# Kernel tuning notes

Measured on AMD Instinct MI355X. Metric: run time of the kernel, lower is better.

The kernel has to match this reference:

```python
import jax, jax.numpy as jnp
import numpy as np
import math

SPARSITY = 0.95


def _linear(x, W, b):
    # torch nn.Linear: y = x @ W.T + b, W is [out, in]
    return jnp.einsum('bsd,od->bso', x, W) + b


def setup_inputs() -> dict:
    key = jax.random.key(0)
    ks = jax.random.split(key, 11)
    B, S, D = 2, 4096, 512
    std = 1.0 / math.sqrt(D)
    inp = {
        'x': jax.random.normal(ks[0], (B, S, D), dtype=jnp.float32),
        'mask_rand': jax.random.uniform(ks[1], (B, S, S), dtype=jnp.float32),
        'Wq': jax.random.normal(ks[2], (D, D), dtype=jnp.float32) * std,
        'bq': jax.random.normal(ks[3], (D,), dtype=jnp.float32) * std,
        'Wk': jax.random.normal(ks[4], (D, D), dtype=jnp.float32) * std,
        'bk': jax.random.normal(ks[5], (D,), dtype=jnp.float32) * std,
        'Wv': jax.random.normal(ks[6], (D, D), dtype=jnp.float32) * std,
        'bv': jax.random.normal(ks[7], (D,), dtype=jnp.float32) * std,
        'Wo': jax.random.normal(ks[8], (D, D), dtype=jnp.float32) * std,
        'bo': jax.random.normal(ks[9], (D,), dtype=jnp.float32) * std,
    }
    return inp


def reference(x, mask_rand, Wq, bq, Wk, bk, Wv, bv, Wo, bo):
    B, S, D = x.shape
    Q = _linear(x, Wq, bq)
    K = _linear(x, Wk, bk)
    V = _linear(x, Wv, bv)
    scores = jnp.einsum('bqd,bkd->bqk', Q, K) / jnp.sqrt(jnp.asarray(D, x.dtype))
    keep = mask_rand > SPARSITY  # random sparsity mask
    sparse_scores = jnp.where(keep, scores, -jnp.inf)
    attn = jax.nn.softmax(sparse_scores, axis=-1)
    attn_out = jnp.einsum('bqk,bkd->bqd', attn, V)
    # faithful to torch: transpose(1,2).contiguous().view(B, S, D)
    attn_out = jnp.swapaxes(attn_out, 1, 2).reshape(B, S, D)
    return _linear(attn_out, Wo, bo)
```

## Files before the change

### kernel.cpp

```cpp
#include <hip/hip_runtime.h>
#include <hip/hip_bf16.h>
#include <math.h>

typedef __bf16 bf16_t;
typedef __attribute__((ext_vector_type(8))) __bf16 bf16x8;
typedef __attribute__((ext_vector_type(4))) float f32x4;

constexpr int B_ = 2, S_ = 4096, D_ = 512;
constexpr int BS_ = B_ * S_;

__device__ __forceinline__ void load16_lds(const bf16_t* g, bf16_t* l) {
    __builtin_amdgcn_global_load_lds(
        (const __attribute__((address_space(1))) void*)g,
        (__attribute__((address_space(3))) void*)l, 16, 0, 0);
}

__global__ __launch_bounds__(256) void cvt_to_bf16(
    const float* __restrict__ src, bf16_t* __restrict__ dst, long n)
{
    const long i = ((long)blockIdx.x * 256 + threadIdx.x) * 4;
    if (i >= n) return;
    const float4 v = *(const float4*)(src + i);
    dst[i + 0] = (bf16_t)v.x;
    dst[i + 1] = (bf16_t)v.y;
    dst[i + 2] = (bf16_t)v.z;
    dst[i + 3] = (bf16_t)v.w;
}

__global__ __launch_bounds__(256) void qkv_gemm(
    const bf16_t* __restrict__ X,
    const bf16_t* __restrict__ Wq, const bf16_t* __restrict__ Wk, const bf16_t* __restrict__ Wv,
    const float* __restrict__ bq, const float* __restrict__ bk, const float* __restrict__ bv,
    bf16_t* __restrict__ Q, bf16_t* __restrict__ Kout, bf16_t* __restrict__ V)
{
    constexpr int K = 512, N = 512;
    const int sel = blockIdx.x >> 2;
    const bf16_t* B = (sel == 0) ? Wq : (sel == 1) ? Wk : Wv;
    const float* bias = (sel == 0) ? bq : (sel == 1) ? bk : bv;
    bf16_t* C = (sel == 0) ? Q : (sel == 1) ? Kout : V;

    __shared__ bf16_t As[128 * 32];
    __shared__ bf16_t Bs[128 * 32];

    const int tid  = threadIdx.x;
    const int wave = tid >> 6;
    const int lane = tid & 63;
    const int quad = lane >> 4;
    const int r16  = lane & 15;
    const int wr   = wave >> 1;
    const int wc   = wave & 1;

    const int m0 = blockIdx.y * 128;
    const int n0 = (blockIdx.x & 3) * 128;

    const int srow = tid >> 2;
    const int scol = (tid & 3) * 8;

    const bf16_t* gA0 = X + (long)(m0 + srow) * K + scol;
    const bf16_t* gA1 = gA0 + (long)64 * K;
    const bf16_t* gB0 = B + (long)(n0 + srow) * K + scol;
    const bf16_t* gB1 = gB0 + (long)64 * K;
    bf16_t* lA = As + tid * 8;
    bf16_t* lB = Bs + tid * 8;

    f32x4 acc[4][4] = {};

    for (int k0 = 0; k0 < K; k0 += 32) {
        load16_lds(gA0 + k0, lA);
        load16_lds(gA1 + k0, lA + 2048);
        load16_lds(gB0 + k0, lB);
        load16_lds(gB1 + k0, lB + 2048);
        __syncthreads();

        bf16x8 af[4], bfr[4];
#pragma unroll
        for (int i = 0; i < 4; i++)
            af[i] = *(const bf16x8*)(As + (wr * 64 + i * 16 + r16) * 32 + quad * 8);
#pragma unroll
        for (int j = 0; j < 4; j++)
            bfr[j] = *(const bf16x8*)(Bs + (wc * 64 + j * 16 + r16) * 32 + quad * 8);

#pragma unroll
        for (int i = 0; i < 4; i++)
#pragma unroll
            for (int j = 0; j < 4; j++)
                acc[i][j] = __builtin_amdgcn_mfma_f32_16x16x32_bf16(af[i], bfr[j], acc[i][j], 0, 0, 0);
        __syncthreads();
    }

#pragma unroll
    for (int i = 0; i < 4; i++) {
#pragma unroll
        for (int j = 0; j < 4; j++) {
            const int gn = n0 + wc * 64 + j * 16 + r16;
            const float bval = bias[gn];
#pragma unroll
            for (int reg = 0; reg < 4; reg++) {
                const int gm = m0 + wr * 64 + i * 16 + quad * 4 + reg;
                C[(long)gm * N + gn] = (bf16_t)(acc[i][j][reg] + bval);
            }
        }
    }
}

__global__ __launch_bounds__(256) void scores_gemm(
    const bf16_t* __restrict__ Q, const bf16_t* __restrict__ Km,
    const float* __restrict__ mask, bf16_t* __restrict__ SC,
    float* __restrict__ rowsum, float scale)
{
    constexpr int S = S_, K = D_;
    const int b = blockIdx.z;
    const bf16_t* A = Q + (long)b * S * K;
    const bf16_t* Bm = Km + (long)b * S * K;

    __shared__ char smem[16384];
    bf16_t* As = (bf16_t*)smem;
    bf16_t* Bs = (bf16_t*)(smem + 8192);

    const int tid  = threadIdx.x;
    const int wave = tid >> 6;
    const int lane = tid & 63;
    const int quad = lane >> 4;
    const int r16  = lane & 15;
    const int wr   = wave >> 1;
    const int wc   = wave & 1;

    const int m0 = blockIdx.y * 128;
    const int n0 = blockIdx.x * 128;

    const int srow = tid >> 2;
    const int scol = (tid & 3) * 8;

    const bf16_t* gA0 = A + (long)(m0 + srow) * K + scol;
    const bf16_t* gA1 = gA0 + (long)64 * K;
    const bf16_t* gB0 = Bm + (long)(n0 + srow) * K + scol;
    const bf16_t* gB1 = gB0 + (long)64 * K;
    bf16_t* lA = As + tid * 8;
    bf16_t* lB = Bs + tid * 8;

    f32x4 acc[4][4] = {};

    for (int k0 = 0; k0 < K; k0 += 32) {
        load16_lds(gA0 + k0, lA);
        load16_lds(gA1 + k0, lA + 2048);
        load16_lds(gB0 + k0, lB);
        load16_lds(gB1 + k0, lB + 2048);
        __syncthreads();

        bf16x8 af[4], bfr[4];
#pragma unroll
        for (int i = 0; i < 4; i++)
            af[i] = *(const bf16x8*)(As + (wr * 64 + i * 16 + r16) * 32 + quad * 8);
#pragma unroll
        for (int j = 0; j < 4; j++)
            bfr[j] = *(const bf16x8*)(Bs + (wc * 64 + j * 16 + r16) * 32 + quad * 8);

#pragma unroll
        for (int i = 0; i < 4; i++)
#pragma unroll
            for (int j = 0; j < 4; j++)
                acc[i][j] = __builtin_amdgcn_mfma_f32_16x16x32_bf16(af[i], bfr[j], acc[i][j], 0, 0, 0);
        __syncthreads();
    }

    float* wlds = (float*)smem + wave * 1024;
    const int erow = lane >> 2;
    const int ecg  = lane & 3;
    const long mbase = (long)b * S * S;

#pragma unroll
    for (int i = 0; i < 4; i++) {
#pragma unroll
        for (int j = 0; j < 4; j++)
#pragma unroll
            for (int reg = 0; reg < 4; reg++)
                wlds[(quad * 4 + reg) * 64 + j * 16 + r16] = acc[i][j][reg];
        __syncthreads();

        float v[16];
#pragma unroll
        for (int c = 0; c < 4; c++) {
            const float4 t = *(const float4*)(wlds + erow * 64 + ecg * 16 + c * 4);
            v[c * 4 + 0] = t.x; v[c * 4 + 1] = t.y;
            v[c * 4 + 2] = t.z; v[c * 4 + 3] = t.w;
        }

        const int gm = m0 + wr * 64 + i * 16 + erow;
        const int gn = n0 + wc * 64 + ecg * 16;
        const float* mp = mask + mbase + (long)gm * S + gn;

        float e[16];
        float rsum = 0.f;
#pragma unroll
        for (int c = 0; c < 4; c++) {
            const float4 mk = *(const float4*)(mp + c * 4);
            e[c * 4 + 0] = (mk.x > 0.95f) ? __expf(v[c * 4 + 0] * scale) : 0.f;
            e[c * 4 + 1] = (mk.y > 0.95f) ? __expf(v[c * 4 + 1] * scale) : 0.f;
            e[c * 4 + 2] = (mk.z > 0.95f) ? __expf(v[c * 4 + 2] * scale) : 0.f;
            e[c * 4 + 3] = (mk.w > 0.95f) ? __expf(v[c * 4 + 3] * scale) : 0.f;
        }
        bf16x8 o0, o1;
#pragma unroll
        for (int t = 0; t < 8; t++) {
            rsum += e[t] + e[t + 8];
            o0[t] = (bf16_t)e[t];
            o1[t] = (bf16_t)e[t + 8];
        }
        bf16_t* cp = SC + mbase + (long)gm * S + gn;
        *(bf16x8*)cp       = o0;
        *(bf16x8*)(cp + 8) = o1;

        rsum += __shfl_xor(rsum, 1, 64);
        rsum += __shfl_xor(rsum, 2, 64);
        if (ecg == 0) atomicAdd(&rowsum[b * S + gm], rsum);
        __syncthreads();
    }
}

template <int PMODE, int KS>
__global__ __launch_bounds__(256) void pv_gemm(
    const bf16_t* __restrict__ VT, const bf16_t* __restrict__ SC,
    const float* __restrict__ rowsum, void* __restrict__ outp)
{
    constexpr int S = S_, D = D_;
    constexpr int KC = S / KS;
    const int z  = blockIdx.z;
    const int b  = z / KS;
    const int ks = z % KS;

    const bf16_t* A  = VT + (long)b * D * S;
    const bf16_t* Bm = SC + (long)b * S * S;

    __shared__ bf16_t As[128 * 32];
    __shared__ bf16_t Bs[128 * 32];

    const int tid  = threadIdx.x;
    const int wave = tid >> 6;
    const int lane = tid & 63;
    const int quad = lane >> 4;
    const int r16  = lane & 15;
    const int wr   = wave >> 1;
    const int wc   = wave & 1;

    const int m0 = blockIdx.y * 128;
    const int n0 = blockIdx.x * 128;

    const int srow = tid >> 2;
    const int scol = (tid & 3) * 8;

    const bf16_t* gA0 = A + (long)(m0 + srow) * S + scol;
    const bf16_t* gA1 = gA0 + (long)64 * S;
    const bf16_t* gB0 = Bm + (long)(n0 + srow) * S + scol;
    const bf16_t* gB1 = gB0 + (long)64 * S;
    bf16_t* lA = As + tid * 8;
    bf16_t* lB = Bs + tid * 8;

    f32x4 acc[4][4] = {};

    const int kbeg = ks * KC;
    const int kend = kbeg + KC;
    for (int k0 = kbeg; k0 < kend; k0 += 32) {
        load16_lds(gA0 + k0, lA);
        load16_lds(gA1 + k0, lA + 2048);
        load16_lds(gB0 + k0, lB);
        load16_lds(gB1 + k0, lB + 2048);
        __syncthreads();

        bf16x8 af[4], bfr[4];
#pragma unroll
        for (int i = 0; i < 4; i++)
            af[i] = *(const bf16x8*)(As + (wr * 64 + i * 16 + r16) * 32 + quad * 8);
#pragma unroll
        for (int j = 0; j < 4; j++)
            bfr[j] = *(const bf16x8*)(Bs + (wc * 64 + j * 16 + r16) * 32 + quad * 8);

#pragma unroll
        for (int i = 0; i < 4; i++)
#pragma unroll
            for (int j = 0; j < 4; j++)
                acc[i][j] = __builtin_amdgcn_mfma_f32_16x16x32_bf16(af[i], bfr[j], acc[i][j], 0, 0, 0);
        __syncthreads();
    }

    const long obase = (PMODE == 2) ? (long)b * D * S
                                    : ((long)ks * B_ + b) * (long)D * S;
#pragma unroll
    for (int i = 0; i < 4; i++) {
#pragma unroll
        for (int j = 0; j < 4; j++) {
            const int gn = n0 + wc * 64 + j * 16 + r16;
            float inv = 1.f;
            if (PMODE == 2) inv = 1.f / rowsum[b * S + gn];
#pragma unroll
            for (int reg = 0; reg < 4; reg++) {
                const int gm = m0 + wr * 64 + i * 16 + quad * 4 + reg;
                const long cidx = obase + (long)gm * S + gn;
                const float v = acc[i][j][reg];
                if (PMODE == 0) ((float*)outp)[cidx]  = v;
                if (PMODE == 1) ((bf16_t*)outp)[cidx] = (bf16_t)v;
                if (PMODE == 2) ((bf16_t*)outp)[cidx] = (bf16_t)(v * inv);
            }
        }
    }
}

template <typename PT, int KS>
__global__ __launch_bounds__(256) void reduce_norm(
    const PT* __restrict__ part, const float* __restrict__ rowsum,
    bf16_t* __restrict__ T)
{
    constexpr long TOT = (long)B_ * D_ * S_;
    constexpr long STR = TOT;
    const long i = ((long)blockIdx.x * 256 + threadIdx.x) * 4;
    if (i >= TOT) return;

    float s[4] = {0.f, 0.f, 0.f, 0.f};
#pragma unroll
    for (int ks = 0; ks < KS; ks++) {
        const PT* p = part + ks * STR + i;
#pragma unroll
        for (int t = 0; t < 4; t++) s[t] += (float)p[t];
    }
    const int b = (int)(i / ((long)D_ * S_));
    const int q = (int)(i & (S_ - 1));
    const float4 rs = *(const float4*)(rowsum + b * S_ + q);
    bf16_t o[4];
    o[0] = (bf16_t)(s[0] / rs.x);
    o[1] = (bf16_t)(s[1] / rs.y);
    o[2] = (bf16_t)(s[2] / rs.z);
    o[3] = (bf16_t)(s[3] / rs.w);
    *(uint2*)(T + i) = *(uint2*)o;
}

__global__ __launch_bounds__(256) void out_gemm(
    const bf16_t* __restrict__ A, const bf16_t* __restrict__ B,
    const float* __restrict__ bias, float* __restrict__ C)
{
    constexpr int N = 512, K = 512;

    __shared__ bf16_t As[128 * 32];
    __shared__ bf16_t Bs[128 * 32];

    const int tid  = threadIdx.x;
    const int wave = tid >> 6;
    const int lane = tid & 63;
    const int quad = lane >> 4;
    const int r16  = lane & 15;
    const int wr   = wave >> 1;
    const int wc   = wave & 1;

    const int m0 = blockIdx.y * 128;
    const int n0 = blockIdx.x * 128;

    const int srow = tid >> 2;
    const int scol = (tid & 3) * 8;

    const bf16_t* gA0 = A + (long)(m0 + srow) * K + scol;
    const bf16_t* gA1 = gA0 + (long)64 * K;
    const bf16_t* gB0 = B + (long)(n0 + srow) * K + scol;
    const bf16_t* gB1 = gB0 + (long)64 * K;
    bf16_t* lA = As + tid * 8;
    bf16_t* lB = Bs + tid * 8;

    f32x4 acc[4][4] = {};

    for (int k0 = 0; k0 < K; k0 += 32) {
        load16_lds(gA0 + k0, lA);
        load16_lds(gA1 + k0, lA + 2048);
        load16_lds(gB0 + k0, lB);
        load16_lds(gB1 + k0, lB + 2048);
        __syncthreads();

        bf16x8 af[4], bfr[4];
#pragma unroll
        for (int i = 0; i < 4; i++)
            af[i] = *(const bf16x8*)(As + (wr * 64 + i * 16 + r16) * 32 + quad * 8);
#pragma unroll
        for (int j = 0; j < 4; j++)
            bfr[j] = *(const bf16x8*)(Bs + (wc * 64 + j * 16 + r16) * 32 + quad * 8);

#pragma unroll
        for (int i = 0; i < 4; i++)
#pragma unroll
            for (int j = 0; j < 4; j++)
                acc[i][j] = __builtin_amdgcn_mfma_f32_16x16x32_bf16(af[i], bfr[j], acc[i][j], 0, 0, 0);
        __syncthreads();
    }

#pragma unroll
    for (int i = 0; i < 4; i++) {
#pragma unroll
        for (int j = 0; j < 4; j++) {
            const int gn = n0 + wc * 64 + j * 16 + r16;
            const float bval = bias[gn];
#pragma unroll
            for (int reg = 0; reg < 4; reg++) {
                const int gm = m0 + wr * 64 + i * 16 + quad * 4 + reg;
                C[(long)gm * N + gn] = acc[i][j][reg] + bval;
            }
        }
    }
}

__global__ __launch_bounds__(256) void transpose_k(
    const bf16_t* __restrict__ in, bf16_t* __restrict__ out, int rows, int cols)
{
    __shared__ bf16_t tile[32][33];
    const int b = blockIdx.z;
    in  += (long)b * rows * cols;
    out += (long)b * rows * cols;
    const int r0 = blockIdx.y * 32;
    const int c0 = blockIdx.x * 32;
    const int tx = threadIdx.x;
    const int ty = threadIdx.y;
#pragma unroll
    for (int i = 0; i < 4; i++)
        tile[ty + 8 * i][tx] = in[(long)(r0 + ty + 8 * i) * cols + c0 + tx];
    __syncthreads();
#pragma unroll
    for (int i = 0; i < 4; i++)
        out[(long)(c0 + ty + 8 * i) * rows + r0 + tx] = tile[tx][ty + 8 * i];
}

extern "C" void kernel_launch(void* const* d_in, const int* in_sizes, int n_in,
                              void* d_out, int out_size, void* d_ws, size_t ws_size,
                              hipStream_t stream)
{
    constexpr int B = B_, S = S_, D = D_;
    constexpr int BS = BS_;
    constexpr long QKV_ELEMS = (long)BS * D;
    constexpr long W_ELEMS   = (long)D * D;
    constexpr long SC_ELEMS  = (long)BS * S;

    const float* x_raw = (const float*)d_in[0];
    const float* mask  = (const float*)d_in[1];
    const float* Wq    = (const float*)d_in[2];
    const float* bq    = (const float*)d_in[3];
    const float* Wk    = (const float*)d_in[4];
    const float* bk    = (const float*)d_in[5];
    const float* Wv    = (const float*)d_in[6];
    const float* bv    = (const float*)d_in[7];
    const float* Wo    = (const float*)d_in[8];
    const float* bo    = (const float*)d_in[9];

    char* ws = (char*)d_ws;
    bf16_t* SC  = (bf16_t*)ws;                       ws += SC_ELEMS * 2;
    bf16_t* VT  = (bf16_t*)ws;                       ws += QKV_ELEMS * 2;
    bf16_t* Q   = (bf16_t*)ws;                       ws += QKV_ELEMS * 2;
    bf16_t* Kp  = (bf16_t*)ws;                       ws += QKV_ELEMS * 2;
    bf16_t* V   = (bf16_t*)ws;                       ws += QKV_ELEMS * 2;
    bf16_t* T   = V;
    bf16_t* Xc  = (bf16_t*)ws;                       ws += QKV_ELEMS * 2;
    bf16_t* Wqc = (bf16_t*)ws;                       ws += W_ELEMS * 2;
    bf16_t* Wkc = (bf16_t*)ws;                       ws += W_ELEMS * 2;
    bf16_t* Wvc = (bf16_t*)ws;                       ws += W_ELEMS * 2;
    bf16_t* Woc = (bf16_t*)ws;                       ws += W_ELEMS * 2;
    float*  rowsum = (float*)ws;                     ws += (long)BS * 4;
    void*   part = (void*)ws;
    const size_t used_base = (size_t)(ws - (char*)d_ws);
    constexpr long PART_ELEMS = 4L * B_ * D_ * S_;
    const int tier = (ws_size >= used_base + PART_ELEMS * 4) ? 0
                   : (ws_size >= used_base + PART_ELEMS * 2) ? 1 : 2;

    const float scale = 0.044194173824159216f;
    dim3 blk(256);

    cvt_to_bf16<<<dim3((int)(QKV_ELEMS / 1024)), blk, 0, stream>>>(x_raw, Xc, QKV_ELEMS);
    cvt_to_bf16<<<dim3((int)(W_ELEMS / 1024)), blk, 0, stream>>>(Wq, Wqc, W_ELEMS);
    cvt_to_bf16<<<dim3((int)(W_ELEMS / 1024)), blk, 0, stream>>>(Wk, Wkc, W_ELEMS);
    cvt_to_bf16<<<dim3((int)(W_ELEMS / 1024)), blk, 0, stream>>>(Wv, Wvc, W_ELEMS);
    cvt_to_bf16<<<dim3((int)(W_ELEMS / 1024)), blk, 0, stream>>>(Wo, Woc, W_ELEMS);

    qkv_gemm<<<dim3(12, 64), blk, 0, stream>>>(Xc, Wqc, Wkc, Wvc, bq, bk, bv, Q, Kp, V);

    transpose_k<<<dim3(D / 32, S / 32, B), dim3(32, 8), 0, stream>>>(V, VT, S, D);

    hipMemsetAsync(rowsum, 0, (long)BS * 4, stream);
    scores_gemm<<<dim3(S / 128, S / 128, B), blk, 0, stream>>>(Q, Kp, mask, SC, rowsum, scale);

    if (tier == 0) {
        pv_gemm<0, 4><<<dim3(S / 128, D / 128, B * 4), blk, 0, stream>>>(VT, SC, rowsum, part);
        reduce_norm<float, 4><<<dim3((int)(QKV_ELEMS / 1024)), blk, 0, stream>>>(
            (const float*)part, rowsum, T);
    } else if (tier == 1) {
        pv_gemm<1, 4><<<dim3(S / 128, D / 128, B * 4), blk, 0, stream>>>(VT, SC, rowsum, part);
        reduce_norm<bf16_t, 4><<<dim3((int)(QKV_ELEMS / 1024)), blk, 0, stream>>>(
            (const bf16_t*)part, rowsum, T);
    } else {
        pv_gemm<2, 1><<<dim3(S / 128, D / 128, B), blk, 0, stream>>>(VT, SC, rowsum, T);
    }

    out_gemm<<<dim3(4, 64), blk, 0, stream>>>(T, Woc, bo, (float*)d_out);
}
```

Before: 395.0 us.

## Pack mask to bytes, fuse input conversions, use bf16 pre-normalized PV partials

The five fp32-to-bf16 conversion launches are merged into one kernel. A new pre-pass packs the fp32 random mask into a byte mask, so the scores kernel reads one byte per element instead of four. When workspace allows, PV split-K partials are normalized by the row sums inside the GEMM and stored as bf16, which halves partial-buffer traffic compared with the old fp32 path. The tradeoff is that the mask packing pass still reads the full fp32 mask and writes an extra byte buffer, so total memory traffic may not drop. Rounding normalized partials to bf16 before summing also slightly changes numerics.

```diff
diff --git a/kernel.cpp b/kernel.cpp
--- a/kernel.cpp
+++ b/kernel.cpp
@@ -15,16 +15,42 @@
         (__attribute__((address_space(3))) void*)l, 16, 0, 0);
 }
 
-__global__ __launch_bounds__(256) void cvt_to_bf16(
-    const float* __restrict__ src, bf16_t* __restrict__ dst, long n)
-{
+__global__ __launch_bounds__(256) void cvt_all(
+    const float* __restrict__ x, const float* __restrict__ Wq,
+    const float* __restrict__ Wk, const float* __restrict__ Wv,
+    const float* __restrict__ Wo, bf16_t* __restrict__ dst)
+{
+    constexpr long QKV = (long)BS_ * D_;
+    constexpr long WE  = (long)D_ * D_;
     const long i = ((long)blockIdx.x * 256 + threadIdx.x) * 4;
-    if (i >= n) return;
-    const float4 v = *(const float4*)(src + i);
-    dst[i + 0] = (bf16_t)v.x;
-    dst[i + 1] = (bf16_t)v.y;
-    dst[i + 2] = (bf16_t)v.z;
-    dst[i + 3] = (bf16_t)v.w;
+    const float* src;
+    long o;
+    if (i < QKV) { src = x; o = i; }
+    else {
+        const long j = i - QKV;
+        const int w = (int)(j >> 18);
+        o = j & (WE - 1);
+        src = (w == 0) ? Wq : (w == 1) ? Wk : (w == 2) ? Wv : Wo;
+    }
+    const float4 v = *(const float4*)(src + o);
+    bf16_t out[4] = {(bf16_t)v.x, (bf16_t)v.y, (bf16_t)v.z, (bf16_t)v.w};
+    *(uint2*)(dst + i) = *(uint2*)out;
+}
+
+__global__ __launch_bounds__(256) void pack_mask(
+    const float* __restrict__ mask, unsigned char* __restrict__ bm)
+{
+    const long i = ((long)blockIdx.x * 256 + threadIdx.x) * 16;
+    unsigned char o[16];
+#pragma unroll
+    for (int c = 0; c < 4; c++) {
+        const float4 v = *(const float4*)(mask + i + c * 4);
+        o[c * 4 + 0] = v.x > 0.95f;
+        o[c * 4 + 1] = v.y > 0.95f;
+        o[c * 4 + 2] = v.z > 0.95f;
+        o[c * 4 + 3] = v.w > 0.95f;
+    }
+    *(uint4*)(bm + i) = *(uint4*)o;
 }
 
 __global__ __launch_bounds__(256) void qkv_gemm(
@@ -103,9 +129,10 @@
     }
 }
 
+template <typename MT>
 __global__ __launch_bounds__(256) void scores_gemm(
     const bf16_t* __restrict__ Q, const bf16_t* __restrict__ Km,
-    const float* __restrict__ mask, bf16_t* __restrict__ SC,
+    const MT* __restrict__ mask, bf16_t* __restrict__ SC,
     float* __restrict__ rowsum, float scale)
 {
     constexpr int S = S_, K = D_;
@@ -187,19 +214,28 @@
 
         const int gm = m0 + wr * 64 + i * 16 + erow;
         const int gn = n0 + wc * 64 + ecg * 16;
-        const float* mp = mask + mbase + (long)gm * S + gn;
 
         float e[16];
+        if (sizeof(MT) == 1) {
+            const uint4 mb = *(const uint4*)((const unsigned char*)mask + mbase + (long)gm * S + gn);
+            const unsigned char* mk = (const unsigned char*)&mb;
+#pragma unroll
+            for (int t = 0; t < 16; t++)
+                e[t] = mk[t] ? __expf(v[t] * scale) : 0.f;
+        } else {
+            const float* mp = (const float*)mask + mbase + (long)gm * S + gn;
+#pragma unroll
+            for (int c = 0; c < 4; c++) {
+                const float4 mk = *(const float4*)(mp + c * 4);
+                e[c * 4 + 0] = (mk.x > 0.95f) ? __expf(v[c * 4 + 0] * scale) : 0.f;
+                e[c * 4 + 1] = (mk.y > 0.95f) ? __expf(v[c * 4 + 1] * scale) : 0.f;
+                e[c * 4 + 2] = (mk.z > 0.95f) ? __expf(v[c * 4 + 2] * scale) : 0.f;
+                e[c * 4 + 3] = (mk.w > 0.95f) ? __expf(v[c * 4 + 3] * scale) : 0.f;
+            }
+        }
+
+        bf16x8 o0, o1;
         float rsum = 0.f;
-#pragma unroll
-        for (int c = 0; c < 4; c++) {
-            const float4 mk = *(const float4*)(mp + c * 4);
-            e[c * 4 + 0] = (mk.x > 0.95f) ? __expf(v[c * 4 + 0] * scale) : 0.f;
-            e[c * 4 + 1] = (mk.y > 0.95f) ? __expf(v[c * 4 + 1] * scale) : 0.f;
-            e[c * 4 + 2] = (mk.z > 0.95f) ? __expf(v[c * 4 + 2] * scale) : 0.f;
-            e[c * 4 + 3] = (mk.w > 0.95f) ? __expf(v[c * 4 + 3] * scale) : 0.f;
-        }
-        bf16x8 o0, o1;
 #pragma unroll
         for (int t = 0; t < 8; t++) {
             rsum += e[t] + e[t + 8];
@@ -290,45 +326,49 @@
         for (int j = 0; j < 4; j++) {
             const int gn = n0 + wc * 64 + j * 16 + r16;
             float inv = 1.f;
-            if (PMODE == 2) inv = 1.f / rowsum[b * S + gn];
+            if (PMODE == 2 || PMODE == 3) inv = 1.f / rowsum[b * S + gn];
 #pragma unroll
             for (int reg = 0; reg < 4; reg++) {
                 const int gm = m0 + wr * 64 + i * 16 + quad * 4 + reg;
                 const long cidx = obase + (long)gm * S + gn;
                 const float v = acc[i][j][reg];
                 if (PMODE == 0) ((float*)outp)[cidx]  = v;
-                if (PMODE == 1) ((bf16_t*)outp)[cidx] = (bf16_t)v;
                 if (PMODE == 2) ((bf16_t*)outp)[cidx] = (bf16_t)(v * inv);
+                if (PMODE == 3) ((bf16_t*)outp)[cidx] = (bf16_t)(v * inv);
             }
         }
     }
 }
 
-template <typename PT, int KS>
-__global__ __launch_bounds__(256) void reduce_norm(
+template <typename PT, int KS, int NORM>
+__global__ __launch_bounds__(256) void reduce_k(
     const PT* __restrict__ part, const float* __restrict__ rowsum,
     bf16_t* __restrict__ T)
 {
     constexpr long TOT = (long)B_ * D_ * S_;
-    constexpr long STR = TOT;
     const long i = ((long)blockIdx.x * 256 + threadIdx.x) * 4;
     if (i >= TOT) return;
 
     float s[4] = {0.f, 0.f, 0.f, 0.f};
 #pragma unroll
     for (int ks = 0; ks < KS; ks++) {
-        const PT* p = part + ks * STR + i;
+        const PT* p = part + ks * TOT + i;
 #pragma unroll
         for (int t = 0; t < 4; t++) s[t] += (float)p[t];
     }
-    const int b = (int)(i / ((long)D_ * S_));
-    const int q = (int)(i & (S_ - 1));
-    const float4 rs = *(const float4*)(rowsum + b * S_ + q);
     bf16_t o[4];
-    o[0] = (bf16_t)(s[0] / rs.x);
-    o[1] = (bf16_t)(s[1] / rs.y);
-    o[2] = (bf16_t)(s[2] / rs.z);
-    o[3] = (bf16_t)(s[3] / rs.w);
+    if (NORM) {
+        const int b = (int)(i / ((long)D_ * S_));
+        const int q = (int)(i & (S_ - 1));
+        const float4 rs = *(const float4*)(rowsum + b * S_ + q);
+        o[0] = (bf16_t)(s[0] / rs.x);
+        o[1] = (bf16_t)(s[1] / rs.y);
+        o[2] = (bf16_t)(s[2] / rs.z);
+        o[3] = (bf16_t)(s[3] / rs.w);
+    } else {
+        o[0] = (bf16_t)s[0]; o[1] = (bf16_t)s[1];
+        o[2] = (bf16_t)s[2]; o[3] = (bf16_t)s[3];
+    }
     *(uint2*)(T + i) = *(uint2*)o;
 }
 
@@ -431,6 +471,7 @@
     constexpr long QKV_ELEMS = (long)BS * D;
     constexpr long W_ELEMS   = (long)D * D;
     constexpr long SC_ELEMS  = (long)BS * S;
+    constexpr long MASK_N    = (long)BS * S;
 
     const float* x_raw = (const float*)d_in[0];
     const float* mask  = (const float*)d_in[1];
@@ -456,36 +497,43 @@
     bf16_t* Wvc = (bf16_t*)ws;                       ws += W_ELEMS * 2;
     bf16_t* Woc = (bf16_t*)ws;                       ws += W_ELEMS * 2;
     float*  rowsum = (float*)ws;                     ws += (long)BS * 4;
-    void*   part = (void*)ws;
+    unsigned char* bmask = (unsigned char*)ws;
+    void* part = (void*)ws;
     const size_t used_base = (size_t)(ws - (char*)d_ws);
+
     constexpr long PART_ELEMS = 4L * B_ * D_ * S_;
-    const int tier = (ws_size >= used_base + PART_ELEMS * 4) ? 0
-                   : (ws_size >= used_base + PART_ELEMS * 2) ? 1 : 2;
+    const int path = (ws_size >= used_base + MASK_N) ? 0
+                   : (ws_size >= used_base + PART_ELEMS * 4) ? 1 : 2;
 
     const float scale = 0.044194173824159216f;
     dim3 blk(256);
 
-    cvt_to_bf16<<<dim3((int)(QKV_ELEMS / 1024)), blk, 0, stream>>>(x_raw, Xc, QKV_ELEMS);
-    cvt_to_bf16<<<dim3((int)(W_ELEMS / 1024)), blk, 0, stream>>>(Wq, Wqc, W_ELEMS);
-    cvt_to_bf16<<<dim3((int)(W_ELEMS / 1024)), blk, 0, stream>>>(Wk, Wkc, W_ELEMS);
-    cvt_to_bf16<<<dim3((int)(W_ELEMS / 1024)), blk, 0, stream>>>(Wv, Wvc, W_ELEMS);
-    cvt_to_bf16<<<dim3((int)(W_ELEMS / 1024)), blk, 0, stream>>>(Wo, Woc, W_ELEMS);
+    cvt_all<<<dim3((int)((QKV_ELEMS + 4 * W_ELEMS) / 1024)), blk, 0, stream>>>(
+        x_raw, Wq, Wk, Wv, Wo, Xc);
+
+    if (path == 0)
+        pack_mask<<<dim3((int)(MASK_N / 4096)), blk, 0, stream>>>(mask, bmask);
 
     qkv_gemm<<<dim3(12, 64), blk, 0, stream>>>(Xc, Wqc, Wkc, Wvc, bq, bk, bv, Q, Kp, V);
 
     transpose_k<<<dim3(D / 32, S / 32, B), dim3(32, 8), 0, stream>>>(V, VT, S, D);
 
     hipMemsetAsync(rowsum, 0, (long)BS * 4, stream);
-    scores_gemm<<<dim3(S / 128, S / 128, B), blk, 0, stream>>>(Q, Kp, mask, SC, rowsum, scale);
-
-    if (tier == 0) {
+    if (path == 0)
+        scores_gemm<unsigned char><<<dim3(S / 128, S / 128, B), blk, 0, stream>>>(
+            Q, Kp, bmask, SC, rowsum, scale);
+    else
+        scores_gemm<float><<<dim3(S / 128, S / 128, B), blk, 0, stream>>>(
+            Q, Kp, mask, SC, rowsum, scale);
+
+    if (path == 0) {
+        pv_gemm<3, 4><<<dim3(S / 128, D / 128, B * 4), blk, 0, stream>>>(VT, SC, rowsum, part);
+        reduce_k<bf16_t, 4, 0><<<dim3((int)(QKV_ELEMS / 1024)), blk, 0, stream>>>(
+            (const bf16_t*)part, rowsum, T);
+    } else if (path == 1) {
         pv_gemm<0, 4><<<dim3(S / 128, D / 128, B * 4), blk, 0, stream>>>(VT, SC, rowsum, part);
-        reduce_norm<float, 4><<<dim3((int)(QKV_ELEMS / 1024)), blk, 0, stream>>>(
+        reduce_k<float, 4, 1><<<dim3((int)(QKV_ELEMS / 1024)), blk, 0, stream>>>(
             (const float*)part, rowsum, T);
-    } else if (tier == 1) {
-        pv_gemm<1, 4><<<dim3(S / 128, D / 128, B * 4), blk, 0, stream>>>(VT, SC, rowsum, part);
-        reduce_norm<bf16_t, 4><<<dim3((int)(QKV_ELEMS / 1024)), blk, 0, stream>>>(
-            (const bf16_t*)part, rowsum, T);
     } else {
         pv_gemm<2, 1><<<dim3(S / 128, D / 128, B), blk, 0, stream>>>(VT, SC, rowsum, T);
     }
```

New measurement: 394.2 us. No clear change (-0.2%).
